# Kernel optimization log

Measured on AMD Instinct MI355X. Metric: run time of the kernel, lower is better.

Reference implementation:

```python
import jax, jax.numpy as jnp
import numpy as np

BINS = 10  # module init arg


def setup_inputs() -> dict:
    key = jax.random.key(0)
    k1, k2 = jax.random.split(key)
    pred = jax.random.normal(k1, (16384, 4096), dtype=jnp.float32)
    target = jax.random.bernoulli(k2, 0.5, (16384, 4096)).astype(jnp.float32)
    return {"pred": pred, "target": target}


def reference(pred, target):
    bins = BINS
    # gradient-norm proxy; sigmoid(pred) is detached in the original
    g = jnp.abs(jax.lax.stop_gradient(jax.nn.sigmoid(pred)) - target)
    tot = jnp.float32(g.size)
    # edges[i] = i/bins with edges[-1] += 1e-6, so bin index = floor(g*bins)
    # clipped to [0, bins-1] (g == 1.0 lands in the last bin).
    idx = jnp.clip(jnp.floor(g * bins).astype(jnp.int32), 0, bins - 1)
    counts = jnp.zeros((bins,), jnp.float32).at[idx.reshape(-1)].add(1.0)
    n = jnp.sum(counts > 0).astype(jnp.float32)  # number of non-empty bins
    per_bin_w = jnp.where(counts > 0, tot / jnp.maximum(counts, 1.0), 0.0)
    weights = per_bin_w[idx] / jnp.maximum(n, 1.0)
    weights = jax.lax.stop_gradient(weights)  # weights carry no grad in torch
    # numerically stable BCE-with-logits, per element
    x, t = pred, target
    bce = jnp.maximum(x, 0.0) - x * t + jnp.log1p(jnp.exp(-jnp.abs(x)))
    return jnp.sum(weights * bce) / tot
```

## Files before the change

### kernel.cpp

```cpp
#include <hip/hip_runtime.h>

#define NBINS 10
#define BLOCK 256
#define GRID  1024
#define NWAVE (BLOCK / 64)

static_assert(BLOCK * 16 == 0x1000, "per-phase step literal must equal BLOCK*16");


__global__ void ghm_init(double* gU, unsigned* gC) {
    int t = threadIdx.x;
    if (t < NBINS) { gU[t] = 0.0; gC[t] = 0u; }
}

#define THRA(TS, AJ)                                                          \
    "v_cmp_le_f32 vcc, " TS ", v40\n\t"                                       \
    "v_cndmask_b32 v45, 0, v44, vcc\n\t"                                      \
    "v_add_u32 " AJ ", " AJ ", v45\n\t"

#define ELEM_ASM(PX, TX)                                                      \
    "v_fma_f32 v40, " TX ", -2.0, 1.0\n\t"              \
    "v_mul_f32 v40, " PX ", v40\n\t"                                  \
    "v_mul_f32 v41, %[nl2e], abs(v40)\n\t"               \
    "v_exp_f32 v42, v41\n\t"                                    \
    "v_max_f32 v43, 0, v40\n\t"                           \
    "v_add_f32 v41, 1.0, v42\n\t"                               \
    "v_log_f32 v41, v41\n\t"                                \
    "v_cmp_le_f32 vcc, %[tau0], v40\n\t"      \
    "v_fma_f32 v43, %[ln2], v41, v43\n\t"                            \
    "v_fma_f32 v44, %[kq], v43, 0.5\n\t"                    \
    "v_cvt_u32_f32 v44, v44\n\t"                                     \
    "v_add_u32 v44, 0x1000000, v44\n\t"              \
    "v_add_u32 %[u0], %[u0], v44\n\t"                              \
    "v_cndmask_b32 v45, 0, v44, vcc\n\t"                                      \
    "v_add_u32 %[a0], %[a0], v45\n\t"                                         \
    THRA("%[tau1]", "%[a1]")                                                  \
    THRA("%[tau2]", "%[a2]")                                                  \
    THRA("%[tau3]", "%[a3]")                                                  \
    THRA("0",       "%[a4]")                                                  \
    THRA("%[tau5]", "%[a5]")                                                  \
    THRA("%[tau6]", "%[a6]")                                                  \
    THRA("%[tau7]", "%[a7]")                                                  \
    THRA("%[tau8]", "%[a8]")

#define QUADC(P0,P1,P2,P3,T0,T1,T2,T3)                                        \
    ELEM_ASM(P0,T0) ELEM_ASM(P1,T1) ELEM_ASM(P2,T2) ELEM_ASM(P3,T3)

#define QUAD_A QUADC("v48","v49","v50","v51","v52","v53","v54","v55")
#define QUAD_B QUADC("v56","v57","v58","v59","v60","v61","v62","v63")
#define QUAD_C QUADC("v64","v65","v66","v67","v68","v69","v70","v71")
#define QUAD_D QUADC("v72","v73","v74","v75","v76","v77","v78","v79")

#define ISSUE_S(SP, ST)                                                       \
    "global_load_dwordx4 " SP ", %[off], %[pb] sc0\n\t"                       \
    "global_load_dwordx4 " ST ", %[off], %[tb] nt\n\t"                        \
    "v_add_u32 %[off], 0x1000, %[off]\n\t"

#define ISSUE_A ISSUE_S("v[48:51]", "v[52:55]")
#define ISSUE_B ISSUE_S("v[56:59]", "v[60:63]")
#define ISSUE_C ISSUE_S("v[64:67]", "v[68:71]")
#define ISSUE_D ISSUE_S("v[72:75]", "v[76:79]")

__global__ __launch_bounds__(BLOCK, 4) void ghm_main(const float4* __restrict__ pred,
                                                     const float4* __restrict__ targ,
                                                     int n4,
                                                     double* __restrict__ gU,
                                                     unsigned* __restrict__ gC) {
    const float TAUH[9] = {-2.19722458f, -1.38629436f, -0.84729786f, -0.40546511f, 0.0f,
                            0.40546511f,  0.84729786f,  1.38629436f,  2.19722458f};

    unsigned Sfx[NBINS];
    unsigned Cnt[NBINS];
#pragma unroll
    for (int j = 0; j < NBINS; ++j) { Sfx[j] = 0u; Cnt[j] = 0u; }

    const int perBlock = n4 / GRID;
    const int P = perBlock / BLOCK;

    if ((n4 % (GRID * BLOCK)) == 0 && P >= 8 && (P % 8) == 0) {
        const unsigned regionBase = (unsigned)blockIdx.x * (unsigned)perBlock * 16u;
        const unsigned tbase = regionBase + (unsigned)threadIdx.x * 16u;
        const int r = 8 * (int)(blockIdx.x % (unsigned)(P / 8));

        int runs[2] = {P - r, r};
        int p0 = r;
        for (int q = 0; q < 2; ++q) {
            int run = runs[q];
            if (q == 1) p0 = 0;
            while (run > 0) {
                int L = run > 32 ? 32 : run;
                unsigned off = tbase + (unsigned)p0 * 4096u;
                int cnt = (L >> 2) - 1;
                unsigned u0 = 0u, a0 = 0u, a1 = 0u, a2 = 0u, a3 = 0u, a4 = 0u,
                         a5 = 0u, a6 = 0u, a7 = 0u, a8 = 0u;

                asm volatile(
                    ISSUE_A ISSUE_B ISSUE_C ISSUE_D
                    "Lmain_%=:\n\t"
                    "s_waitcnt vmcnt(6)\n\t" QUAD_A ISSUE_A
                    "s_waitcnt vmcnt(6)\n\t" QUAD_B ISSUE_B
                    "s_waitcnt vmcnt(6)\n\t" QUAD_C ISSUE_C
                    "s_waitcnt vmcnt(6)\n\t" QUAD_D ISSUE_D
                    "s_sub_u32 %[cnt], %[cnt], 1\n\t"
                    "s_cmp_lg_u32 %[cnt], 0\n\t"
                    "s_cbranch_scc1 Lmain_%=\n\t"
                    "s_waitcnt vmcnt(6)\n\t" QUAD_A
                    "s_waitcnt vmcnt(4)\n\t" QUAD_B
                    "s_waitcnt vmcnt(2)\n\t" QUAD_C
                    "s_waitcnt vmcnt(0)\n\t" QUAD_D
                    : [u0]"+v"(u0), [a0]"+v"(a0), [a1]"+v"(a1), [a2]"+v"(a2),
                      [a3]"+v"(a3), [a4]"+v"(a4), [a5]"+v"(a5), [a6]"+v"(a6),
                      [a7]"+v"(a7), [a8]"+v"(a8), [off]"+v"(off), [cnt]"+s"(cnt)
                    : [pb]"s"(pred), [tb]"s"(targ),
                      [nl2e]"s"(-1.44269504f), [ln2]"s"(0.69314718f), [kq]"s"(4096.0f),
                      [tau0]"s"(TAUH[0]), [tau1]"s"(TAUH[1]), [tau2]"s"(TAUH[2]),
                      [tau3]"s"(TAUH[3]), [tau5]"s"(TAUH[5]), [tau6]"s"(TAUH[6]),
                      [tau7]"s"(TAUH[7]), [tau8]"s"(TAUH[8])
                    : "vcc", "scc", "memory",
                      "v40","v41","v42","v43","v44","v45",
                      "v48","v49","v50","v51","v52","v53","v54","v55",
                      "v56","v57","v58","v59","v60","v61","v62","v63",
                      "v64","v65","v66","v67","v68","v69","v70","v71",
                      "v72","v73","v74","v75","v76","v77","v78","v79");

                const unsigned elems = (unsigned)(L * 4);
                Sfx[0] += u0 - (elems << 24);  Cnt[0] += elems;
                unsigned aa[9] = {a0,a1,a2,a3,a4,a5,a6,a7,a8};
#pragma unroll
                for (int j = 0; j < 9; ++j) {
                    Sfx[1 + j] += aa[j] & 0xFFFFFFu;
                    Cnt[1 + j] += aa[j] >> 24;
                }
                p0 += L; run -= L;
            }
        }
    } else {
        const int stride = GRID * BLOCK;
        for (int k = blockIdx.x * BLOCK + threadIdx.x; k < n4; k += stride) {
            float4 p = pred[k];
            float4 t = targ[k];
            float px[4] = {p.x, p.y, p.z, p.w};
            float tx[4] = {t.x, t.y, t.z, t.w};
            for (int e = 0; e < 4; ++e) {
                float xp = px[e] * fmaf(-2.0f, tx[e], 1.0f);
                float e2 = __builtin_amdgcn_exp2f(fabsf(xp) * -1.44269504f);
                float bce = fmaf(0.69314718f, __builtin_amdgcn_logf(1.0f + e2),
                                 fmaxf(xp, 0.0f));
                unsigned bfx = (unsigned)(fmaf(4096.0f, bce, 0.5f));
                Sfx[0] += bfx; Cnt[0] += 1u;
#pragma unroll
                for (int j = 0; j < 9; ++j) {
                    bool pg = (xp >= TAUH[j]);
                    Sfx[1 + j] += pg ? bfx : 0u;
                    Cnt[1 + j] += pg ? 1u : 0u;
                }
            }
        }
    }

#pragma unroll
    for (int j = 0; j < NBINS; ++j) {
#pragma unroll
        for (int m = 1; m < 64; m <<= 1) {
            Sfx[j] += (unsigned)__shfl_xor((int)Sfx[j], m, 64);
            Cnt[j] += (unsigned)__shfl_xor((int)Cnt[j], m, 64);
        }
    }

    __shared__ unsigned sS[NWAVE][NBINS];
    __shared__ unsigned sC[NWAVE][NBINS];
    const int wid  = threadIdx.x >> 6;
    const int lane = threadIdx.x & 63;
    if (lane == 0) {
#pragma unroll
        for (int j = 0; j < NBINS; ++j) { sS[wid][j] = Sfx[j]; sC[wid][j] = Cnt[j]; }
    }
    __syncthreads();

    if (threadIdx.x < NBINS) {
        unsigned s = 0u, c = 0u;
#pragma unroll
        for (int w = 0; w < NWAVE; ++w) { s += sS[w][threadIdx.x]; c += sC[w][threadIdx.x]; }
        atomicAdd(&gU[threadIdx.x], (double)s);
        if (threadIdx.x > 0) atomicAdd(&gC[threadIdx.x], c);
    }
}

__global__ void ghm_finalize(const double* __restrict__ gU,
                             const unsigned* __restrict__ gC,
                             float* __restrict__ out, unsigned ntot) {
    if (threadIdx.x == 0 && blockIdx.x == 0) {
        double acc = 0.0;
        int n = 0;
        for (int b = 0; b < NBINS; ++b) {
            double   hiU = (b < 9) ? gU[b + 1] : 0.0;
            unsigned hiC = (b < 9) ? gC[b + 1] : 0u;
            double   S = (gU[b] - hiU) * (1.0 / 4096.0);
            unsigned c = ((b == 0) ? ntot : gC[b]) - hiC;
            if (c > 0u) {
                ++n;
                acc += S / (double)c;
            }
        }
        if (n < 1) n = 1;
        out[0] = (float)(acc / (double)n);
    }
}

extern "C" void kernel_launch(void* const* d_in, const int* in_sizes, int n_in,
                              void* d_out, int out_size, void* d_ws, size_t ws_size,
                              hipStream_t stream) {
    const float4* pred = (const float4*)d_in[0];
    const float4* targ = (const float4*)d_in[1];
    double*   gU = (double*)d_ws;
    unsigned* gC = (unsigned*)((char*)d_ws + NBINS * sizeof(double));
    float* out = (float*)d_out;

    int n4 = in_sizes[0] / 4;
    unsigned ntot = (unsigned)in_sizes[0];

    ghm_init<<<1, 64, 0, stream>>>(gU, gC);
    ghm_main<<<GRID, BLOCK, 0, stream>>>(pred, targ, n4, gU, gC);
    ghm_finalize<<<1, 64, 0, stream>>>(gU, gC, out, ntot);
}
```

Baseline: 93.16 us.

## Deepen target prefetch to eight phases with separate pred/target offsets

The inline-asm streaming loop now keeps eight target vectors in flight (v48–v79) but only four pred vectors (v80–v95). It uses separate offset registers for pred and target and processes eight phases per iteration instead of four. The goal is more outstanding memory loads to hide HBM latency. The cost is 16 more VGPRs, which under launch_bounds(256,4) may still fit. The vmcnt bookkeeping is more intricate, and a wrong count would read stale registers.

Result: slower. 96.30 us (+3.4%).

```diff
diff --git a/kernel.cpp b/kernel.cpp
--- a/kernel.cpp
+++ b/kernel.cpp
@@ -46,20 +46,21 @@
 #define QUADC(P0,P1,P2,P3,T0,T1,T2,T3)                                        \
     ELEM_ASM(P0,T0) ELEM_ASM(P1,T1) ELEM_ASM(P2,T2) ELEM_ASM(P3,T3)
 
-#define QUAD_A QUADC("v48","v49","v50","v51","v52","v53","v54","v55")
-#define QUAD_B QUADC("v56","v57","v58","v59","v60","v61","v62","v63")
-#define QUAD_C QUADC("v64","v65","v66","v67","v68","v69","v70","v71")
-#define QUAD_D QUADC("v72","v73","v74","v75","v76","v77","v78","v79")
-
-#define ISSUE_S(SP, ST)                                                       \
-    "global_load_dwordx4 " SP ", %[off], %[pb] sc0\n\t"                       \
-    "global_load_dwordx4 " ST ", %[off], %[tb] nt\n\t"                        \
-    "v_add_u32 %[off], 0x1000, %[off]\n\t"
-
-#define ISSUE_A ISSUE_S("v[48:51]", "v[52:55]")
-#define ISSUE_B ISSUE_S("v[56:59]", "v[60:63]")
-#define ISSUE_C ISSUE_S("v[64:67]", "v[68:71]")
-#define ISSUE_D ISSUE_S("v[72:75]", "v[76:79]")
+#define PH0 QUADC("v80","v81","v82","v83","v48","v49","v50","v51")
+#define PH1 QUADC("v84","v85","v86","v87","v52","v53","v54","v55")
+#define PH2 QUADC("v88","v89","v90","v91","v56","v57","v58","v59")
+#define PH3 QUADC("v92","v93","v94","v95","v60","v61","v62","v63")
+#define PH4 QUADC("v80","v81","v82","v83","v64","v65","v66","v67")
+#define PH5 QUADC("v84","v85","v86","v87","v68","v69","v70","v71")
+#define PH6 QUADC("v88","v89","v90","v91","v72","v73","v74","v75")
+#define PH7 QUADC("v92","v93","v94","v95","v76","v77","v78","v79")
+
+#define IS_T(REG)                                                             \
+    "global_load_dwordx4 " REG ", %[offT], %[tb] nt\n\t"                      \
+    "v_add_u32 %[offT], 0x1000, %[offT]\n\t"
+#define IS_P(REG)                                                             \
+    "global_load_dwordx4 " REG ", %[offP], %[pb] sc0\n\t"                     \
+    "v_add_u32 %[offP], 0x1000, %[offP]\n\t"
 
 __global__ __launch_bounds__(BLOCK, 4) void ghm_main(const float4* __restrict__ pred,
                                                      const float4* __restrict__ targ,
@@ -89,28 +90,44 @@
             if (q == 1) p0 = 0;
             while (run > 0) {
                 int L = run > 32 ? 32 : run;
-                unsigned off = tbase + (unsigned)p0 * 4096u;
-                int cnt = (L >> 2) - 1;
+                unsigned offT = tbase + (unsigned)p0 * 4096u;
+                unsigned offP = offT;
+                int cnt = (L >> 3) - 1;
                 unsigned u0 = 0u, a0 = 0u, a1 = 0u, a2 = 0u, a3 = 0u, a4 = 0u,
                          a5 = 0u, a6 = 0u, a7 = 0u, a8 = 0u;
 
                 asm volatile(
-                    ISSUE_A ISSUE_B ISSUE_C ISSUE_D
+                    IS_T("v[48:51]") IS_T("v[52:55]") IS_P("v[80:83]")
+                    IS_T("v[56:59]") IS_T("v[60:63]") IS_P("v[84:87]")
+                    IS_T("v[64:67]") IS_T("v[68:71]") IS_P("v[88:91]")
+                    IS_T("v[72:75]") IS_T("v[76:79]") IS_P("v[92:95]")
+                    "s_cmp_eq_u32 %[cnt], 0\n\t"
+                    "s_cbranch_scc1 Lepi_%=\n\t"
                     "Lmain_%=:\n\t"
-                    "s_waitcnt vmcnt(6)\n\t" QUAD_A ISSUE_A
-                    "s_waitcnt vmcnt(6)\n\t" QUAD_B ISSUE_B
-                    "s_waitcnt vmcnt(6)\n\t" QUAD_C ISSUE_C
-                    "s_waitcnt vmcnt(6)\n\t" QUAD_D ISSUE_D
+                    "s_waitcnt vmcnt(6)\n\t" PH0 IS_T("v[48:51]") IS_P("v[80:83]")
+                    "s_waitcnt vmcnt(6)\n\t" PH1 IS_T("v[52:55]") IS_P("v[84:87]")
+                    "s_waitcnt vmcnt(6)\n\t" PH2 IS_T("v[56:59]") IS_P("v[88:91]")
+                    "s_waitcnt vmcnt(6)\n\t" PH3 IS_T("v[60:63]") IS_P("v[92:95]")
+                    "s_waitcnt vmcnt(6)\n\t" PH4 IS_T("v[64:67]") IS_P("v[80:83]")
+                    "s_waitcnt vmcnt(6)\n\t" PH5 IS_T("v[68:71]") IS_P("v[84:87]")
+                    "s_waitcnt vmcnt(6)\n\t" PH6 IS_T("v[72:75]") IS_P("v[88:91]")
+                    "s_waitcnt vmcnt(6)\n\t" PH7 IS_T("v[76:79]") IS_P("v[92:95]")
                     "s_sub_u32 %[cnt], %[cnt], 1\n\t"
                     "s_cmp_lg_u32 %[cnt], 0\n\t"
                     "s_cbranch_scc1 Lmain_%=\n\t"
-                    "s_waitcnt vmcnt(6)\n\t" QUAD_A
-                    "s_waitcnt vmcnt(4)\n\t" QUAD_B
-                    "s_waitcnt vmcnt(2)\n\t" QUAD_C
-                    "s_waitcnt vmcnt(0)\n\t" QUAD_D
+                    "Lepi_%=:\n\t"
+                    "s_waitcnt vmcnt(6)\n\t" PH0 IS_P("v[80:83]")
+                    "s_waitcnt vmcnt(5)\n\t" PH1 IS_P("v[84:87]")
+                    "s_waitcnt vmcnt(4)\n\t" PH2 IS_P("v[88:91]")
+                    "s_waitcnt vmcnt(3)\n\t" PH3 IS_P("v[92:95]")
+                    "s_waitcnt vmcnt(3)\n\t" PH4
+                    "s_waitcnt vmcnt(2)\n\t" PH5
+                    "s_waitcnt vmcnt(1)\n\t" PH6
+                    "s_waitcnt vmcnt(0)\n\t" PH7
                     : [u0]"+v"(u0), [a0]"+v"(a0), [a1]"+v"(a1), [a2]"+v"(a2),
                       [a3]"+v"(a3), [a4]"+v"(a4), [a5]"+v"(a5), [a6]"+v"(a6),
-                      [a7]"+v"(a7), [a8]"+v"(a8), [off]"+v"(off), [cnt]"+s"(cnt)
+                      [a7]"+v"(a7), [a8]"+v"(a8),
+                      [offT]"+v"(offT), [offP]"+v"(offP), [cnt]"+s"(cnt)
                     : [pb]"s"(pred), [tb]"s"(targ),
                       [nl2e]"s"(-1.44269504f), [ln2]"s"(0.69314718f), [kq]"s"(4096.0f),
                       [tau0]"s"(TAUH[0]), [tau1]"s"(TAUH[1]), [tau2]"s"(TAUH[2]),
@@ -121,7 +138,9 @@
                       "v48","v49","v50","v51","v52","v53","v54","v55",
                       "v56","v57","v58","v59","v60","v61","v62","v63",
                       "v64","v65","v66","v67","v68","v69","v70","v71",
-                      "v72","v73","v74","v75","v76","v77","v78","v79");
+                      "v72","v73","v74","v75","v76","v77","v78","v79",
+                      "v80","v81","v82","v83","v84","v85","v86","v87",
+                      "v88","v89","v90","v91","v92","v93","v94","v95");
 
                 const unsigned elems = (unsigned)(L * 4);
                 Sfx[0] += u0 - (elems << 24);  Cnt[0] += elems;
```
